# Kernel optimization log

Measured on AMD Instinct MI355X. Metric: run time of the kernel, lower is better.

The kernel has to match this reference:

```python
import jax, jax.numpy as jnp
import numpy as np

N_SP = 2      # zero out the N smallest-magnitude entries...
M_SP = 4      # ...per group of M features (2:4 activation sparsity)
Q_MAX = 127.0  # 2**(8-1) - 1 for 8-bit symmetric quant


def setup_inputs() -> dict:
    key = jax.random.key(0)
    k1, k2, k3 = jax.random.split(key, 3)
    B, S, DIN, DOUT = 4, 2048, 4096, 4096
    x = jax.random.normal(k1, (B, S, DIN), dtype=jnp.float32)
    # weight buffer is randn in __init__ (out_features, in_features)
    weight = jax.random.normal(k2, (DOUT, DIN), dtype=jnp.float32) * 0.02
    bias = jnp.zeros((1, DOUT), dtype=jnp.float32)
    # sparsity_scale = per-column weight-norm ratio >= 1 (see from_float)
    sparsity_scale = jax.random.uniform(k3, (1, DIN), dtype=jnp.float32,
                                        minval=1.0, maxval=4.0)
    return {"x": x, "weight": weight, "bias": bias,
            "sparsity_scale": sparsity_scale}


def _apply_activation_sparsity(x, scale):
    """Zero the N_SP smallest |x|*scale entries in each group of M_SP columns."""
    shp = x.shape
    d = shp[-1]
    x2 = x.reshape(-1, d)                      # (T, d)
    metric = jnp.abs(x2) * scale               # (T, d)
    g = d // M_SP
    mg = metric.reshape(-1, g, M_SP)           # (T, g, m)
    # indices of the n smallest per group (topk largest=False in torch)
    _, idx = jax.lax.top_k(-mg, N_SP)          # (T, g, n)
    # mask[t, g, j] = True if j is one of the n smallest in its group
    mask = (idx[..., :, None] == jnp.arange(M_SP)[None, None, None, :]).any(axis=-2)
    mask = mask.reshape(-1, d)
    return jnp.where(mask, jnp.zeros((), x2.dtype), x2).reshape(shp)


def _quant_per_token_absmax(t):
    scales = jnp.max(jnp.abs(t), axis=-1, keepdims=True)
    scales = jnp.clip(scales, 1e-5, None) / Q_MAX
    return jnp.round(t / scales) * scales


def reference(x, weight, bias, sparsity_scale):
    # pre_quant 2:4 activation sparsity
    xs = _apply_activation_sparsity(x, sparsity_scale)
    # per-token absmax fake-quant of activations
    qx = _quant_per_token_absmax(xs)
    # dense linear: y = qx @ W^T + b  (output_quant is identity)
    y = jnp.einsum('bsi,oi->bso', qx, weight) + bias
    return y
```

## Files before the change

### kernel.cpp

```cpp
#include <hip/hip_runtime.h>
#include <hip/hip_bf16.h>
#include <stdint.h>

#define T_TOK 8192
#define K_DIM 4096
#define N_DIM 4096
#define NT 64

typedef short bf16x8 __attribute__((ext_vector_type(8)));
typedef float f32x4  __attribute__((ext_vector_type(4)));
typedef __attribute__((address_space(3))) char* ldsptr;

__device__ __forceinline__ unsigned short f2bf(float f) {
    uint32_t u = __float_as_uint(f);
    u += 0x7FFFu + ((u >> 16) & 1u);
    return (unsigned short)(u >> 16);
}

__device__ __forceinline__ void gl16(const unsigned short* g, ldsptr l) {
    __builtin_amdgcn_global_load_lds(
        (const __attribute__((address_space(1))) void*)g,
        (__attribute__((address_space(3))) void*)l, 16, 0, 0);
}

__global__ __launch_bounds__(256) void wconv_kernel(const float* __restrict__ w,
                                                    unsigned short* __restrict__ wb) {
    int i = (blockIdx.x * 256 + threadIdx.x) * 4;
    float4 v = *(const float4*)(w + i);
    ushort4 o;
    o.x = f2bf(v.x); o.y = f2bf(v.y); o.z = f2bf(v.z); o.w = f2bf(v.w);
    *(ushort4*)(wb + i) = o;
}

__global__ __launch_bounds__(256) void sparsequant_kernel(
        const float* __restrict__ x, const float* __restrict__ ss,
        unsigned short* __restrict__ qi, float* __restrict__ scales) {
    const int row = blockIdx.x;
    const int t = threadIdx.x;
    const float* xr = x + (size_t)row * K_DIM;

    float xs[16];
    float amax = 0.f;
#pragma unroll
    for (int j = 0; j < 4; ++j) {
        int g = t + 256 * j;
        float4 v  = ((const float4*)xr)[g];
        float4 sv = ((const float4*)ss)[g];
        float e[4] = { v.x, v.y, v.z, v.w };
        float m[4] = { fabsf(v.x) * sv.x, fabsf(v.y) * sv.y,
                       fabsf(v.z) * sv.z, fabsf(v.w) * sv.w };
#pragma unroll
        for (int a = 0; a < 4; ++a) {
            int cnt = 0;
#pragma unroll
            for (int b = 0; b < 4; ++b) {
                if (b == a) continue;
                bool less = (m[b] < m[a]) || (m[b] == m[a] && b < a);
                cnt += less ? 1 : 0;
            }
            float kept = (cnt >= 2) ? e[a] : 0.f;
            xs[j * 4 + a] = kept;
            amax = fmaxf(amax, fabsf(kept));
        }
    }
#pragma unroll
    for (int off = 32; off >= 1; off >>= 1)
        amax = fmaxf(amax, __shfl_xor(amax, off, 64));
    __shared__ float wm[4];
    int wave = t >> 6, lane = t & 63;
    if (lane == 0) wm[wave] = amax;
    __syncthreads();
    amax = fmaxf(fmaxf(wm[0], wm[1]), fmaxf(wm[2], wm[3]));

    float s = fmaxf(amax, 1e-5f) / 127.0f;
    if (t == 0) scales[row] = s;

    unsigned short* qr = qi + (size_t)row * K_DIM;
#pragma unroll
    for (int j = 0; j < 4; ++j) {
        int g = t + 256 * j;
        ushort4 o;
        o.x = f2bf(rintf(xs[j * 4 + 0] / s));
        o.y = f2bf(rintf(xs[j * 4 + 1] / s));
        o.z = f2bf(rintf(xs[j * 4 + 2] / s));
        o.w = f2bf(rintf(xs[j * 4 + 3] / s));
        ((ushort4*)qr)[g] = o;
    }
}


#define LREAD(dst, base, imm) \
    asm volatile("ds_read_b128 %0, %1 offset:%2" : "=v"(dst) : "v"(base), "i"(imm))

#define STAGE_A(T, H, BUF) do {                                                  \
    const unsigned short* g_ = pa + (size_t)(H) * 128 * K_DIM + (size_t)(T) * 64;\
    gl16(g_,                      smem3 + ((BUF) * 32768 + (H) * 16384) + tid * 16);          \
    gl16(g_ + (size_t)64 * K_DIM, smem3 + ((BUF) * 32768 + (H) * 16384 + 8192) + tid * 16);   \
} while (0)

#define STAGE_B(T, H, BUF) do {                                                  \
    const unsigned short* g_ = pb + (size_t)(H) * 128 * K_DIM + (size_t)(T) * 64;\
    gl16(g_,                      smem3 + (65536 + (BUF) * 32768 + (H) * 16384) + tid * 16);        \
    gl16(g_ + (size_t)64 * K_DIM, smem3 + (65536 + (BUF) * 32768 + (H) * 16384 + 8192) + tid * 16); \
} while (0)

#define PHASE_TAIL(HA, HB, BFARR) do {                                           \
    __builtin_amdgcn_s_barrier();                                                \
    asm volatile("s_waitcnt lgkmcnt(0)" ::: "memory");                           \
    __builtin_amdgcn_sched_barrier(0);   \
    __builtin_amdgcn_s_setprio(1);                                               \
    _Pragma("unroll")                                                            \
    for (int s_ = 0; s_ < 2; ++s_)                                               \
      _Pragma("unroll")                                                          \
      for (int i_ = 0; i_ < 4; ++i_)                                             \
        _Pragma("unroll")                                                        \
        for (int j_ = 0; j_ < 2; ++j_)                                           \
          acc[HA][i_][HB][j_] = __builtin_amdgcn_mfma_f32_16x16x32_bf16(         \
              af[i_][s_], BFARR[j_][s_], acc[HA][i_][HB][j_], 0, 0, 0);          \
    __builtin_amdgcn_s_setprio(0);                                               \
} while (0)

#define TILE_STEP(T, BUF, SA1, SB1, SA0, SB0, VMC) do {                          \
          \
    _Pragma("unroll")                                                            \
    for (int i_ = 0; i_ < 4; ++i_) {                                             \
        LREAD(af[i_][0], aB, (BUF) * 32768 + (i_ * 2 + 0) * 1024);               \
        LREAD(af[i_][1], aB, (BUF) * 32768 + (i_ * 2 + 1) * 1024);               \
    }                                                                            \
    _Pragma("unroll")                                                            \
    for (int j_ = 0; j_ < 2; ++j_) {                                             \
        LREAD(bf0[j_][0], bB, (BUF) * 32768 + (j_ * 2 + 0) * 1024);              \
        LREAD(bf0[j_][1], bB, (BUF) * 32768 + (j_ * 2 + 1) * 1024);              \
    }                                                                            \
    if (SA1) STAGE_A((T) + 1, 1, (BUF) ^ 1);                                     \
    PHASE_TAIL(0, 0, bf0);                                                       \
    __builtin_amdgcn_s_barrier();                                                \
                       \
    _Pragma("unroll")                                                            \
    for (int j_ = 0; j_ < 2; ++j_) {                                             \
        LREAD(bf1[j_][0], bB, (BUF) * 32768 + 16384 + (j_ * 2 + 0) * 1024);      \
        LREAD(bf1[j_][1], bB, (BUF) * 32768 + 16384 + (j_ * 2 + 1) * 1024);      \
    }                                                                            \
    if (SB1) STAGE_B((T) + 1, 1, (BUF) ^ 1);                                     \
    PHASE_TAIL(0, 1, bf1);                                                       \
    __builtin_amdgcn_s_barrier();                                                \
                          \
    _Pragma("unroll")                                                            \
    for (int i_ = 0; i_ < 4; ++i_) {                                             \
        LREAD(af[i_][0], aB, (BUF) * 32768 + 16384 + (i_ * 2 + 0) * 1024);       \
        LREAD(af[i_][1], aB, (BUF) * 32768 + 16384 + (i_ * 2 + 1) * 1024);       \
    }                                                                            \
    if (SA0) STAGE_A((T) + 2, 0, (BUF));                                         \
    PHASE_TAIL(1, 0, bf0);                                                       \
    __builtin_amdgcn_s_barrier();                                                \
      \
    if (SB0) STAGE_B((T) + 2, 0, (BUF));                                         \
    PHASE_TAIL(1, 1, bf1);                                                       \
    asm volatile("s_waitcnt vmcnt(%0)" :: "i"(VMC) : "memory");                  \
    __builtin_amdgcn_s_barrier();                                                \
} while (0)

__global__ __launch_bounds__(512, 2) void gemm256_kernel(
        const unsigned short* __restrict__ A,
        const unsigned short* __restrict__ B,
        const float* __restrict__ scales,
        const float* __restrict__ bias,
        float* __restrict__ C) {
    extern __shared__ char smem[];
    ldsptr smem3 = (ldsptr)smem;

    const int tid = threadIdx.x;

    const int wg  = blockIdx.x;
    const int swz = (wg & 7) * 64 + (wg >> 3);
    const int tn  = swz >> 5;
    const int tm  = swz & 31;
    const int tmBase = tm * 256, tnBase = tn * 256;

    const int st0  = tid >> 6;
    const int r16s = (tid >> 2) & 15;
    const int q4   = tid & 3;
    const int r0   = ((st0 >> 1) << 4) + r16s;
    const int kk0  = ((st0 & 1) << 5) + ((q4 * 8) ^ ((r16s >> 3) << 4));
    const unsigned short* pa = A + (size_t)(tmBase + r0) * K_DIM + kk0;
    const unsigned short* pb = B + (size_t)(tnBase + r0) * K_DIM + kk0;

    const int lane = tid & 63, wave = tid >> 6;
    const int wr = wave >> 2, wc = wave & 3;
    const int laneoff = (lane & 15) * 64 +
        ((((lane >> 4) * 8) ^ (((lane >> 3) & 1) << 4)) << 1);
    ldsptr aB = smem3 + wr * 8192 + laneoff;
    ldsptr bB = smem3 + 65536 + wc * 4096 + laneoff;

    bf16x8 af[4][2], bf0[2][2], bf1[2][2];
    f32x4 acc[2][4][2][2];
    const f32x4 z = { 0.f, 0.f, 0.f, 0.f };
#pragma unroll
    for (int a0 = 0; a0 < 2; ++a0)
#pragma unroll
      for (int a1 = 0; a1 < 4; ++a1)
#pragma unroll
        for (int a2 = 0; a2 < 2; ++a2)
#pragma unroll
          for (int a3 = 0; a3 < 2; ++a3) acc[a0][a1][a2][a3] = z;

    STAGE_A(0, 0, 0); STAGE_B(0, 0, 0); STAGE_A(0, 1, 0); STAGE_B(0, 1, 0);
    STAGE_A(1, 0, 1); STAGE_B(1, 0, 1);
    asm volatile("s_waitcnt vmcnt(4)" ::: "memory");
    __builtin_amdgcn_s_barrier();

    for (int t = 0; t < NT - 2; t += 2) {
        TILE_STEP(t,     0, 1, 1, 1, 1, 4);
        TILE_STEP(t + 1, 1, 1, 1, 1, 1, 4);
    }
    TILE_STEP(NT - 2, 0, 1, 1, 0, 0, 0);
    TILE_STEP(NT - 1, 1, 0, 0, 0, 0, 0);

#pragma unroll
    for (int ha = 0; ha < 2; ++ha)
#pragma unroll
      for (int i = 0; i < 4; ++i) {
        const int rbase = tmBase + ha * 128 + wr * 64 + i * 16 + (lane >> 4) * 4;
        float sc[4];
#pragma unroll
        for (int r = 0; r < 4; ++r) sc[r] = scales[rbase + r];
#pragma unroll
        for (int hb = 0; hb < 2; ++hb)
#pragma unroll
          for (int j = 0; j < 2; ++j) {
            const int col = tnBase + hb * 128 + wc * 32 + j * 16 + (lane & 15);
            const float bb = bias[col];
#pragma unroll
            for (int r = 0; r < 4; ++r)
                C[(size_t)(rbase + r) * N_DIM + col] = sc[r] * acc[ha][i][hb][j][r] + bb;
          }
      }
}

extern "C" void kernel_launch(void* const* d_in, const int* in_sizes, int n_in,
                              void* d_out, int out_size, void* d_ws, size_t ws_size,
                              hipStream_t stream) {
    const float* x    = (const float*)d_in[0];
    const float* w    = (const float*)d_in[1];
    const float* bias = (const float*)d_in[2];
    const float* ss   = (const float*)d_in[3];
    float* out = (float*)d_out;

    unsigned short* qi = (unsigned short*)d_ws;
    float* scales = (float*)((char*)d_ws + (size_t)T_TOK * K_DIM * 2);
    unsigned short* wb = (unsigned short*)((char*)d_ws + (size_t)T_TOK * K_DIM * 2 + T_TOK * 4);

    wconv_kernel<<<(N_DIM * K_DIM) / (256 * 4), 256, 0, stream>>>(w, wb);
    sparsequant_kernel<<<T_TOK, 256, 0, stream>>>(x, ss, qi, scales);

    (void)hipFuncSetAttribute(reinterpret_cast<const void*>(gemm256_kernel),
                              hipFuncAttributeMaxDynamicSharedMemorySize, 131072);
    gemm256_kernel<<<dim3(512), dim3(512), 131072, stream>>>(qi, wb, scales, bias, out);
}
```

Before: 517.5 us.

## Software-pipeline LDS fragment reads across GEMM phases with partial lgkmcnt waits

```diff
diff --git a/kernel.cpp b/kernel.cpp
--- a/kernel.cpp
+++ b/kernel.cpp
@@ -92,6 +92,15 @@
 #define LREAD(dst, base, imm) \
     asm volatile("ds_read_b128 %0, %1 offset:%2" : "=v"(dst) : "v"(base), "i"(imm))
 
+#define WAIT_LGKM(N) do {                                           \
+    asm volatile("s_waitcnt lgkmcnt(%0)" :: "i"(N) : "memory");     \
+    __builtin_amdgcn_sched_barrier(0);                \
+} while (0)
+
+#define WAIT_VM(N) asm volatile("s_waitcnt vmcnt(%0)" :: "i"(N) : "memory")
+#define BAR() __builtin_amdgcn_s_barrier()
+#define NOP do {} while (0)
+
 #define STAGE_A(T, H, BUF) do {                                                  \
     const unsigned short* g_ = pa + (size_t)(H) * 128 * K_DIM + (size_t)(T) * 64;\
     gl16(g_,                      smem3 + ((BUF) * 32768 + (H) * 16384) + tid * 16);          \
@@ -104,10 +113,23 @@
     gl16(g_ + (size_t)64 * K_DIM, smem3 + (65536 + (BUF) * 32768 + (H) * 16384 + 8192) + tid * 16); \
 } while (0)
 
-#define PHASE_TAIL(HA, HB, BFARR) do {                                           \
-    __builtin_amdgcn_s_barrier();                                                \
-    asm volatile("s_waitcnt lgkmcnt(0)" ::: "memory");                           \
-    __builtin_amdgcn_sched_barrier(0);   \
+#define READ_AF(BUF, H) do {                                                     \
+    _Pragma("unroll")                                                            \
+    for (int i_ = 0; i_ < 4; ++i_) {                                             \
+        LREAD(af[i_][0], aB, (BUF) * 32768 + (H) * 16384 + (i_ * 2 + 0) * 1024); \
+        LREAD(af[i_][1], aB, (BUF) * 32768 + (H) * 16384 + (i_ * 2 + 1) * 1024); \
+    }                                                                            \
+} while (0)
+
+#define READ_BF(ARR, BUF, H) do {                                                \
+    _Pragma("unroll")                                                            \
+    for (int j_ = 0; j_ < 2; ++j_) {                                             \
+        LREAD(ARR[j_][0], bB, (BUF) * 32768 + (H) * 16384 + (j_ * 2 + 0) * 1024);\
+        LREAD(ARR[j_][1], bB, (BUF) * 32768 + (H) * 16384 + (j_ * 2 + 1) * 1024);\
+    }                                                                            \
+} while (0)
+
+#define MFMA_C(HA, HB, BF) do {                                                  \
     __builtin_amdgcn_s_setprio(1);                                               \
     _Pragma("unroll")                                                            \
     for (int s_ = 0; s_ < 2; ++s_)                                               \
@@ -116,48 +138,37 @@
         _Pragma("unroll")                                                        \
         for (int j_ = 0; j_ < 2; ++j_)                                           \
           acc[HA][i_][HB][j_] = __builtin_amdgcn_mfma_f32_16x16x32_bf16(         \
-              af[i_][s_], BFARR[j_][s_], acc[HA][i_][HB][j_], 0, 0, 0);          \
+              af[i_][s_], BF[j_][s_], acc[HA][i_][HB][j_], 0, 0, 0);             \
     __builtin_amdgcn_s_setprio(0);                                               \
 } while (0)
 
-#define TILE_STEP(T, BUF, SA1, SB1, SA0, SB0, VMC) do {                          \
-          \
-    _Pragma("unroll")                                                            \
-    for (int i_ = 0; i_ < 4; ++i_) {                                             \
-        LREAD(af[i_][0], aB, (BUF) * 32768 + (i_ * 2 + 0) * 1024);               \
-        LREAD(af[i_][1], aB, (BUF) * 32768 + (i_ * 2 + 1) * 1024);               \
-    }                                                                            \
-    _Pragma("unroll")                                                            \
-    for (int j_ = 0; j_ < 2; ++j_) {                                             \
-        LREAD(bf0[j_][0], bB, (BUF) * 32768 + (j_ * 2 + 0) * 1024);              \
-        LREAD(bf0[j_][1], bB, (BUF) * 32768 + (j_ * 2 + 1) * 1024);              \
-    }                                                                            \
-    if (SA1) STAGE_A((T) + 1, 1, (BUF) ^ 1);                                     \
-    PHASE_TAIL(0, 0, bf0);                                                       \
-    __builtin_amdgcn_s_barrier();                                                \
-                       \
-    _Pragma("unroll")                                                            \
-    for (int j_ = 0; j_ < 2; ++j_) {                                             \
-        LREAD(bf1[j_][0], bB, (BUF) * 32768 + 16384 + (j_ * 2 + 0) * 1024);      \
-        LREAD(bf1[j_][1], bB, (BUF) * 32768 + 16384 + (j_ * 2 + 1) * 1024);      \
-    }                                                                            \
-    if (SB1) STAGE_B((T) + 1, 1, (BUF) ^ 1);                                     \
-    PHASE_TAIL(0, 1, bf1);                                                       \
-    __builtin_amdgcn_s_barrier();                                                \
-                          \
-    _Pragma("unroll")                                                            \
-    for (int i_ = 0; i_ < 4; ++i_) {                                             \
-        LREAD(af[i_][0], aB, (BUF) * 32768 + 16384 + (i_ * 2 + 0) * 1024);       \
-        LREAD(af[i_][1], aB, (BUF) * 32768 + 16384 + (i_ * 2 + 1) * 1024);       \
-    }                                                                            \
-    if (SA0) STAGE_A((T) + 2, 0, (BUF));                                         \
-    PHASE_TAIL(1, 0, bf0);                                                       \
-    __builtin_amdgcn_s_barrier();                                                \
-      \
-    if (SB0) STAGE_B((T) + 2, 0, (BUF));                                         \
-    PHASE_TAIL(1, 1, bf1);                                                       \
-    asm volatile("s_waitcnt vmcnt(%0)" :: "i"(VMC) : "memory");                  \
-    __builtin_amdgcn_s_barrier();                                                \
+#define PF_NEXT(NBUF) do { READ_AF(NBUF, 0); READ_BF(bf0, NBUF, 0); } while (0)
+
+#define TILE(BUF, S1, S2, S3, S4, PF, W3, W4) do {                               \
+                                                                  \
+    READ_BF(bf1, BUF, 1);                                                        \
+    S1;                                                                          \
+    WAIT_LGKM(4);                                                                \
+    MFMA_C(0, 0, bf0);                                                           \
+    BAR();                                                                       \
+                                                                  \
+    S2;                                                                          \
+    WAIT_LGKM(0);                                                                \
+    MFMA_C(0, 1, bf1);                                                           \
+    READ_AF(BUF, 1);                                                             \
+    BAR();                                                                       \
+                                                                  \
+    S3;                                                                          \
+    WAIT_LGKM(0);                                                                \
+    MFMA_C(1, 1, bf1);                                                           \
+    W3;                                                                          \
+    BAR();                                                                       \
+                                                                  \
+    S4;                                                                          \
+    MFMA_C(1, 0, bf0);                                                           \
+    PF;                                                                          \
+    W4;                                                                          \
+    BAR();                                                                       \
 } while (0)
 
 __global__ __launch_bounds__(512, 2) void gemm256_kernel(
@@ -206,15 +217,22 @@
 
     STAGE_A(0, 0, 0); STAGE_B(0, 0, 0); STAGE_A(0, 1, 0); STAGE_B(0, 1, 0);
     STAGE_A(1, 0, 1); STAGE_B(1, 0, 1);
-    asm volatile("s_waitcnt vmcnt(4)" ::: "memory");
-    __builtin_amdgcn_s_barrier();
+    WAIT_VM(4);
+    BAR();
+    READ_AF(0, 0);
+    READ_BF(bf0, 0, 0);
 
     for (int t = 0; t < NT - 2; t += 2) {
-        TILE_STEP(t,     0, 1, 1, 1, 1, 4);
-        TILE_STEP(t + 1, 1, 1, 1, 1, 1, 4);
+        TILE(0, STAGE_A(t + 1, 1, 1), STAGE_B(t + 1, 1, 1),
+                STAGE_A(t + 2, 0, 0), STAGE_B(t + 2, 0, 0),
+                PF_NEXT(1), WAIT_VM(6), WAIT_VM(4));
+        TILE(1, STAGE_A(t + 2, 1, 0), STAGE_B(t + 2, 1, 0),
+                STAGE_A(t + 3, 0, 1), STAGE_B(t + 3, 0, 1),
+                PF_NEXT(0), WAIT_VM(6), WAIT_VM(4));
     }
-    TILE_STEP(NT - 2, 0, 1, 1, 0, 0, 0);
-    TILE_STEP(NT - 1, 1, 0, 0, 0, 0, 0);
+    TILE(0, STAGE_A(63, 1, 1), STAGE_B(63, 1, 1), NOP, NOP,
+            PF_NEXT(1), WAIT_VM(4), WAIT_VM(0));
+    TILE(1, NOP, NOP, NOP, NOP, NOP, NOP, NOP);
 
 #pragma unroll
     for (int ha = 0; ha < 2; ++ha)
```

Result: no change. 516.7 us (-0.2%).
